# Optimization experiments

Hardware: AMD Instinct MI355X
Metric: run time of the kernel (lower is better)

The kernel has to match this reference:

```python
import jax, jax.numpy as jnp
import numpy as np

B, T, E, H = 4, 1024, 1024, 16
D = E // H  # head_size = 64
EPS = 1e-5


def layernorm(x, g, b):
    mu = jnp.mean(x, axis=-1, keepdims=True)
    var = jnp.mean(jnp.square(x - mu), axis=-1, keepdims=True)
    return (x - mu) * jax.lax.rsqrt(var + EPS) * g + b


def setup_inputs() -> dict:
    key = jax.random.key(0)
    ks = jax.random.split(key, 12)
    s = 0.02
    return {
        "x": jax.random.normal(ks[0], (B, T, E), dtype=jnp.float32),
        "ln1_g": jnp.ones((E,), jnp.float32),
        "ln1_b": jnp.zeros((E,), jnp.float32),
        "Wq": jax.random.normal(ks[1], (H, E, D), dtype=jnp.float32) * s,
        "Wk": jax.random.normal(ks[2], (H, E, D), dtype=jnp.float32) * s,
        "Wv": jax.random.normal(ks[3], (H, E, D), dtype=jnp.float32) * s,
        "Wp": jax.random.normal(ks[4], (E, E), dtype=jnp.float32) * s,
        "bp": jnp.zeros((E,), jnp.float32),
        "ln2_g": jnp.ones((E,), jnp.float32),
        "ln2_b": jnp.zeros((E,), jnp.float32),
        "W1": jax.random.normal(ks[5], (E, 4 * E), dtype=jnp.float32) * s,
        "b1": jnp.zeros((4 * E,), jnp.float32),
        "W2": jax.random.normal(ks[6], (4 * E, E), dtype=jnp.float32) * s,
        "b2": jnp.zeros((E,), jnp.float32),
    }


def reference(x, ln1_g, ln1_b, Wq, Wk, Wv, Wp, bp, ln2_g, ln2_b, W1, b1, W2, b2):
    # --- attention sub-block (pre-LN) ---
    h = layernorm(x, ln1_g, ln1_b)               # [B,T,E]
    q = jnp.einsum('bte,hed->bhtd', h, Wq)       # [B,H,T,D]
    k = jnp.einsum('bte,hed->bhtd', h, Wk)
    v = jnp.einsum('bte,hed->bhtd', h, Wv)
    # NOTE: original module has NO 1/sqrt(D) scaling and its 'tril' buffer is
    # all-ones, so masked_fill is a no-op -> full (non-causal) softmax.
    scores = jnp.einsum('bhtd,bhsd->bhts', q, k)  # [B,H,T,T]
    attn = jax.nn.softmax(scores, axis=-1)
    o = jnp.einsum('bhts,bhsd->bhtd', attn, v)    # [B,H,T,D]
    o = o.transpose(0, 2, 1, 3).reshape(x.shape[0], x.shape[1], -1)  # [B,T,E]
    x = x + o @ Wp + bp
    # --- feedforward sub-block (dropout is identity at eval) ---
    h2 = layernorm(x, ln2_g, ln2_b)
    x = x + jax.nn.relu(h2 @ W1 + b1) @ W2 + b2
    return x
```

## Files before the change

### kernel.cpp

```cpp
#include <hip/hip_runtime.h>
#include <hip/hip_bf16.h>

#define BB 4
#define TT 1024
#define EE 1024
#define HH 16
#define DD 64
#define MM 4096
#define NQKV 3072
#define E4 4096

using short8  = __attribute__((ext_vector_type(8))) short;
using short4v = __attribute__((ext_vector_type(4))) short;
using f32x4   = __attribute__((ext_vector_type(4))) float;

__device__ __forceinline__ short f2bf(float f) {
    __hip_bfloat16 h = __float2bfloat16(f);
    return *reinterpret_cast<short*>(&h);
}

__device__ __forceinline__ float bf2f(short s) {
    unsigned int u = ((unsigned int)(unsigned short)s) << 16;
    return __uint_as_float(u);
}

__device__ __forceinline__ unsigned int cvtpk_bf16(float a, float b) {
    unsigned int w;
    asm("v_cvt_pk_bf16_f32 %0, %1, %2" : "=v"(w) : "v"(a), "v"(b));
    return w;
}

__device__ __forceinline__ void gld16(const void* g, void* l) {
    __builtin_amdgcn_global_load_lds((__attribute__((address_space(1))) void*)g,
                                     (__attribute__((address_space(3))) void*)l,
                                     16, 0, 0);
}

__device__ __forceinline__ void tcvt_tile(const float* __restrict__ in,
                                          short* __restrict__ out,
                                          int R, int C, int r0, int c0) {
    __shared__ short tile[64][65];
    const int tr = threadIdx.x >> 6;
    const int tc = threadIdx.x & 63;
#pragma unroll
    for (int i = 0; i < 16; ++i) {
        int r = i * 4 + tr;
        tile[tc][r] = f2bf(in[(size_t)(r0 + r) * C + c0 + tc]);
    }
    __syncthreads();
#pragma unroll
    for (int i = 0; i < 16; ++i) {
        int c = i * 4 + tr;
        out[(size_t)(c0 + c) * R + r0 + tc] = tile[c][tc];
    }
}

__global__ __launch_bounds__(256) void packs_kernel(const float* __restrict__ Wq,
                                                    const float* __restrict__ Wk,
                                                    const float* __restrict__ Wv,
                                                    const float* __restrict__ Wp,
                                                    const float* __restrict__ W1,
                                                    const float* __restrict__ W2,
                                                    short* __restrict__ wqkv,
                                                    short* __restrict__ wp_bf,
                                                    short* __restrict__ w1_bf,
                                                    short* __restrict__ w2_bf) {
    const int blk = blockIdx.x;
    if (blk < 768) {
        __shared__ short tile[64][65];
        const int m = blk >> 4;
        const int which = m >> 4, head = m & 15;
        const float* src = ((which == 0) ? Wq : (which == 1) ? Wk : Wv) +
                           (size_t)head * EE * DD;
        const float scale = (which == 1) ? 1.44269504f : 1.0f;
        const int e0 = (blk & 15) * 64;
        const int tr = threadIdx.x >> 6, tc = threadIdx.x & 63;
#pragma unroll
        for (int i = 0; i < 16; ++i) {
            int e = i * 4 + tr;
            tile[tc][e] = f2bf(src[(size_t)(e0 + e) * DD + tc] * scale);
        }
        __syncthreads();
#pragma unroll
        for (int i = 0; i < 16; ++i) {
            int d = i * 4 + tr;
            wqkv[(size_t)(which * 1024 + head * 64 + d) * EE + e0 + tc] = tile[d][tc];
        }
    } else if (blk < 1024) {
        const int idx = blk - 768;
        tcvt_tile(Wp, wp_bf, EE, EE, (idx >> 4) * 64, (idx & 15) * 64);
    } else if (blk < 2048) {
        const int idx = blk - 1024;
        tcvt_tile(W1, w1_bf, EE, E4, (idx >> 6) * 64, (idx & 63) * 64);
    } else {
        const int idx = blk - 2048;
        tcvt_tile(W2, w2_bf, E4, EE, (idx >> 4) * 64, (idx & 15) * 64);
    }
}

__global__ __launch_bounds__(256) void vtr_kernel(const short* __restrict__ qkv,
                                                  short* __restrict__ vT) {
    __shared__ short tile[64][68];
    const int b = blockIdx.z;
    const int t0 = blockIdx.x * 64, c0 = blockIdx.y * 64;
    const int tr = threadIdx.x >> 4;
    const int q4 = (threadIdx.x & 15) * 4;
#pragma unroll
    for (int i = 0; i < 4; ++i) {
        int t = i * 16 + tr;
        short4v v = *(const short4v*)&qkv[((size_t)b * TT + t0 + t) * NQKV + 2048 + c0 + q4];
        *(short4v*)&tile[t][q4] = v;
    }
    __syncthreads();
#pragma unroll
    for (int i = 0; i < 4; ++i) {
        int c = i * 16 + tr;
        short4v v;
        v[0] = tile[q4 + 0][c];
        v[1] = tile[q4 + 1][c];
        v[2] = tile[q4 + 2][c];
        v[3] = tile[q4 + 3][c];
        *(short4v*)&vT[((size_t)b * 1024 + c0 + c) * TT + t0 + q4] = v;
    }
}

__global__ __launch_bounds__(256) void ln_kernel(const float* __restrict__ x,
                                                 const float* __restrict__ g,
                                                 const float* __restrict__ b,
                                                 short* __restrict__ out) {
    __shared__ float red[4];
    const int row = blockIdx.x;
    const int tid = threadIdx.x;
    float4 v = *(const float4*)&x[(size_t)row * EE + tid * 4];
    float s = v.x + v.y + v.z + v.w;
#pragma unroll
    for (int off = 32; off >= 1; off >>= 1) s += __shfl_xor(s, off, 64);
    if ((tid & 63) == 0) red[tid >> 6] = s;
    __syncthreads();
    float mean = (red[0] + red[1] + red[2] + red[3]) * (1.0f / EE);
    __syncthreads();
    float d0 = v.x - mean, d1 = v.y - mean, d2 = v.z - mean, d3 = v.w - mean;
    s = d0 * d0 + d1 * d1 + d2 * d2 + d3 * d3;
#pragma unroll
    for (int off = 32; off >= 1; off >>= 1) s += __shfl_xor(s, off, 64);
    if ((tid & 63) == 0) red[tid >> 6] = s;
    __syncthreads();
    float var = (red[0] + red[1] + red[2] + red[3]) * (1.0f / EE);
    float rstd = rsqrtf(var + 1e-5f);
    int c = tid * 4;
    short4v o;
    o[0] = f2bf(d0 * rstd * g[c + 0] + b[c + 0]);
    o[1] = f2bf(d1 * rstd * g[c + 1] + b[c + 1]);
    o[2] = f2bf(d2 * rstd * g[c + 2] + b[c + 2]);
    o[3] = f2bf(d3 * rstd * g[c + 3] + b[c + 3]);
    *(short4v*)&out[(size_t)row * EE + c] = o;
}

__global__ __launch_bounds__(256) void redk4_kernel(const short* __restrict__ parts,
                                                    const float* __restrict__ bias,
                                                    const float* __restrict__ resid,
                                                    float* __restrict__ out) {
    const size_t i = ((size_t)blockIdx.x * 256 + threadIdx.x) * 4;
    float4 r = *(const float4*)&resid[i];
    float4 bb = *(const float4*)&bias[i & 1023];
    float acc0 = r.x + bb.x, acc1 = r.y + bb.y, acc2 = r.z + bb.z, acc3 = r.w + bb.w;
#pragma unroll
    for (int z = 0; z < 4; ++z) {
        short4v p = *(const short4v*)&parts[(size_t)z * MM * EE + i];
        acc0 += bf2f(p[0]);
        acc1 += bf2f(p[1]);
        acc2 += bf2f(p[2]);
        acc3 += bf2f(p[3]);
    }
    float4 o;
    o.x = acc0; o.y = acc1; o.z = acc2; o.w = acc3;
    *(float4*)&out[i] = o;
}

template <bool HAS_BIAS, bool RELU, bool SPLIT>
__global__ __launch_bounds__(512, 2) void gemm256(const short* __restrict__ A,
                                                  const short* __restrict__ Bt,
                                                  const float* __restrict__ bias,
                                                  void* __restrict__ outp,
                                                  int M, int N, int K, int lda) {
    __shared__ __align__(16) short Ab[2][2][8192];
    __shared__ __align__(16) short Bb[2][2][8192];

    const int tid = threadIdx.x;
    const int lane = tid & 63;
    const int wid = tid >> 6;
    const int wr = wid >> 2;
    const int wc = wid & 3;
    const int l15 = lane & 15, lhi = lane >> 4;
    const int rsw = l15 & 7;

    int wg = blockIdx.y * gridDim.x + blockIdx.x;
    const int chunk = (gridDim.x * gridDim.y) >> 3;
    wg = (wg & 7) * chunk + (wg >> 3);
    const int bx = wg % gridDim.x, by = wg / gridDim.x;
    const int row0 = by * 256, col0 = bx * 256;

    const int kb = SPLIT ? blockIdx.z * K : 0;

    const int srow = tid >> 3;
    const int scol = (((tid & 7) ^ (srow & 7)) << 3);

    const int NT = K >> 6;

    f32x4 acc[8][4] = {};

    auto stageA = [&](int b, int h, int k0) {
#pragma unroll
        for (int j = 0; j < 2; ++j)
            gld16(&A[(size_t)(row0 + h * 128 + j * 64 + srow) * lda + kb + k0 + scol],
                  &Ab[b][h][j * 4096 + wid * 512]);
    };
    auto stageB = [&](int b, int h, int k0) {
#pragma unroll
        for (int j = 0; j < 2; ++j)
            gld16(&Bt[(size_t)(col0 + h * 128 + j * 64 + srow) * lda + kb + k0 + scol],
                  &Bb[b][h][j * 4096 + wid * 512]);
    };

    stageA(0, 0, 0); stageA(0, 1, 0);
    stageB(0, 0, 0); stageB(0, 1, 0);
    if (NT > 1) {
        stageB(1, 0, 64); stageB(1, 1, 64);
        asm volatile("s_waitcnt vmcnt(4)" ::: "memory");
    } else {
        asm volatile("s_waitcnt vmcnt(0)" ::: "memory");
    }
    __builtin_amdgcn_s_barrier();

    for (int u = 0; u < NT; ++u) {
        const int buf = u & 1;
        short8 bfr[4][2];
#pragma unroll
        for (int p = 0; p < 4; ++p) {
            if (p == 0) {
#pragma unroll
                for (int n = 0; n < 4; ++n)
#pragma unroll
                    for (int ks = 0; ks < 2; ++ks)
                        bfr[n][ks] = *(const short8*)&Bb[buf][wc >> 1]
                            [((wc & 1) * 64 + n * 16 + l15) * 64 +
                             (((ks << 2) + lhi) ^ rsw) * 8];
            }
            short8 af[2][2];
#pragma unroll
            for (int mi = 0; mi < 2; ++mi)
#pragma unroll
                for (int ks = 0; ks < 2; ++ks)
                    af[mi][ks] = *(const short8*)&Ab[buf][wr]
                        [((p * 2 + mi) * 16 + l15) * 64 +
                         (((ks << 2) + lhi) ^ rsw) * 8];
            if (p == 0 && u + 1 < NT) stageA(buf ^ 1, 0, (u + 1) << 6);
            if (p == 1 && u + 1 < NT) stageA(buf ^ 1, 1, (u + 1) << 6);
            if (p == 2 && u + 2 < NT) stageB(buf, 0, (u + 2) << 6);
            if (p == 3 && u + 2 < NT) stageB(buf, 1, (u + 2) << 6);
            __builtin_amdgcn_s_barrier();
            __builtin_amdgcn_s_setprio(1);
#pragma unroll
            for (int mi = 0; mi < 2; ++mi)
#pragma unroll
                for (int n = 0; n < 4; ++n)
#pragma unroll
                    for (int ks = 0; ks < 2; ++ks)
                        acc[p * 2 + mi][n] = __builtin_amdgcn_mfma_f32_16x16x32_bf16(
                            af[mi][ks], bfr[n][ks], acc[p * 2 + mi][n], 0, 0, 0);
            __builtin_amdgcn_s_setprio(0);
            if (p == 3 && u + 1 < NT) {
                if (u + 2 < NT) asm volatile("s_waitcnt vmcnt(4)" ::: "memory");
                else            asm volatile("s_waitcnt vmcnt(0)" ::: "memory");
            }
            __builtin_amdgcn_s_barrier();
        }
    }

    short* outb = (short*)outp;
    if (SPLIT) outb += (size_t)blockIdx.z * M * N;
#pragma unroll
    for (int m = 0; m < 8; ++m)
#pragma unroll
        for (int n = 0; n < 4; ++n)
#pragma unroll
            for (int r = 0; r < 4; ++r) {
                int row = row0 + wr * 128 + m * 16 + lhi * 4 + r;
                int col = col0 + wc * 64 + n * 16 + l15;
                float v = acc[m][n][r];
                if (!SPLIT) {
                    if (HAS_BIAS) v += bias[col];
                    if (RELU) v = fmaxf(v, 0.f);
                }
                outb[(size_t)row * N + col] = f2bf(v);
            }
}

template <int BN, int PIPE, bool HAS_BIAS, bool RELU, bool RESID, bool OUT_BF16>
__global__ __launch_bounds__(256) void gemm_bt(const short* __restrict__ A,
                                               const short* __restrict__ Bt,
                                               const float* __restrict__ bias,
                                               const float* __restrict__ resid,
                                               void* __restrict__ outp,
                                               int M, int N, int K) {
    constexpr int WRC = (BN == 128) ? 2 : 4;
    constexpr int WCC = (BN == 128) ? 2 : 1;
    constexpr int MI = 8 / WRC;
    constexpr int NI = BN / (16 * WCC);
    constexpr int BCH = BN / 32;
    constexpr int ASZ = 128 * 64, BSZ = BN * 64;

    __shared__ __align__(16) short As[(PIPE ? 2 : 1) * ASZ];
    __shared__ __align__(16) short Bs[(PIPE ? 2 : 1) * BSZ];

    const int tid = threadIdx.x;
    const int lane = tid & 63;
    const int wid = tid >> 6;
    const int wr = (WRC == 2) ? (wid >> 1) : wid;
    const int wc = (WCC == 2) ? (wid & 1) : 0;
    const int l15 = lane & 15, lhi = lane >> 4;

    int wg = blockIdx.y * gridDim.x + blockIdx.x;
    const int chunk = (gridDim.x * gridDim.y) >> 3;
    wg = (wg & 7) * chunk + (wg >> 3);
    const int bx = wg % gridDim.x;
    const int by = wg / gridDim.x;
    const int row0 = by * 128, col0 = bx * BN;

    const int srow = tid >> 3;
    const int scol = (((tid & 7) ^ (srow & 7)) << 3);
    const int rsw = l15 & 7;

    const int wrow0 = wr * (16 * MI);
    const int wcol0 = wc * (16 * NI);

    f32x4 acc[MI][NI] = {};

    auto stage = [&](int k0, int bs) {
#pragma unroll
        for (int ch = 0; ch < 4; ++ch)
            gld16(&A[(size_t)(row0 + ch * 32 + srow) * K + k0 + scol],
                  &As[bs * ASZ + ch * 2048 + wid * 512]);
#pragma unroll
        for (int ch = 0; ch < BCH; ++ch)
            gld16(&Bt[(size_t)(col0 + ch * 32 + srow) * K + k0 + scol],
                  &Bs[bs * BSZ + ch * 2048 + wid * 512]);
    };
    auto compute = [&](int bs) {
#pragma unroll
        for (int ks = 0; ks < 2; ++ks) {
            short8 af[MI], bf[NI];
#pragma unroll
            for (int mi = 0; mi < MI; ++mi)
                af[mi] = *(const short8*)&As[bs * ASZ + (wrow0 + mi * 16 + l15) * 64 +
                                             (((ks << 2) + lhi) ^ rsw) * 8];
#pragma unroll
            for (int ni = 0; ni < NI; ++ni)
                bf[ni] = *(const short8*)&Bs[bs * BSZ + (wcol0 + ni * 16 + l15) * 64 +
                                             (((ks << 2) + lhi) ^ rsw) * 8];
#pragma unroll
            for (int mi = 0; mi < MI; ++mi)
#pragma unroll
                for (int ni = 0; ni < NI; ++ni)
                    acc[mi][ni] = __builtin_amdgcn_mfma_f32_16x16x32_bf16(
                        af[mi], bf[ni], acc[mi][ni], 0, 0, 0);
        }
    };

    if (PIPE == 1) {
        const int nt = K >> 6;
        stage(0, 0);
        stage(64, 1);
        int cur = 0;
        for (int t = 0; t < nt; ++t) {
            if (t + 1 < nt) asm volatile("s_waitcnt vmcnt(6)" ::: "memory");
            else            asm volatile("s_waitcnt vmcnt(0)" ::: "memory");
            __builtin_amdgcn_s_barrier();
            __builtin_amdgcn_sched_barrier(0);
            compute(cur);
            __builtin_amdgcn_sched_barrier(0);
            __builtin_amdgcn_s_barrier();
            if (t + 2 < nt) stage((t + 2) << 6, cur);
            cur ^= 1;
        }
    } else {
        for (int k0 = 0; k0 < K; k0 += 64) {
            __syncthreads();
            stage(k0, 0);
            __syncthreads();
            compute(0);
        }
    }

    float* outf = (float*)outp;
    short* outb = (short*)outp;
#pragma unroll
    for (int mi = 0; mi < MI; ++mi)
#pragma unroll
        for (int ni = 0; ni < NI; ++ni)
#pragma unroll
            for (int r = 0; r < 4; ++r) {
                int row = row0 + wrow0 + mi * 16 + lhi * 4 + r;
                int col = col0 + wcol0 + ni * 16 + l15;
                float v = acc[mi][ni][r];
                if (HAS_BIAS) v += bias[col];
                if (RELU) v = fmaxf(v, 0.f);
                if (RESID) v += resid[(size_t)row * N + col];
                if (OUT_BF16) outb[(size_t)row * N + col] = f2bf(v);
                else outf[(size_t)row * N + col] = v;
            }
}

__global__ __launch_bounds__(512) void attn_kernel(const short* __restrict__ qkv,
                                                   const short* __restrict__ vT,
                                                   short* __restrict__ obuf) {
    __shared__ __align__(16) short Ks[2][128 * 64];
    __shared__ __align__(16) short Vs[2][64 * 128];
    __shared__ __align__(16) unsigned int Pl[8][16][44];
    const int tid = threadIdx.x;
    const int lane = tid & 63;
    const int wid = tid >> 6;
    const int l15 = lane & 15, lhi = lane >> 4;
    const int lhi4 = lhi * 4;

    const int nb = ((blockIdx.x & 7) << 5) + (blockIdx.x >> 3);
    const int b = nb >> 6;
    const int h = (nb >> 2) & 15;
    const int q0 = (nb & 3) << 8;
    const size_t rbase = (size_t)b * TT;
    const int hq = h * 64;
    const short* vg = vT + ((size_t)b * 1024 + hq) * TT;

    const int srow = tid >> 3;
    const int scol = (((tid & 7) ^ (srow & 7)) << 3);
    const int vrow = tid >> 4;
    const int vscol = ((tid & 15) ^ (vrow & 7)) << 3;
    const int rsw = l15 & 7;

    short8 aq[2][2];
#pragma unroll
    for (int g = 0; g < 2; ++g)
#pragma unroll
        for (int ks = 0; ks < 2; ++ks)
            aq[g][ks] = *(const short8*)&qkv[(rbase + q0 + wid * 32 + g * 16 + l15) * NQKV +
                                             hq + ks * 32 + lhi * 8];

    f32x4 psum[2] = {};
    f32x4 o[2][4] = {};

    auto stage = [&](int buf, int st) {
#pragma unroll
        for (int ch = 0; ch < 2; ++ch)
            gld16(&qkv[(rbase + st + ch * 64 + srow) * NQKV + 1024 + hq + scol],
                  &Ks[buf][ch * 4096 + wid * 512]);
#pragma unroll
        for (int ch = 0; ch < 2; ++ch)
            gld16(&vg[(size_t)(ch * 32 + vrow) * TT + st + vscol],
                  &Vs[buf][ch * 4096 + wid * 512]);
    };

    stage(0, 0);
    __syncthreads();

    int cur = 0;
    for (int st = 0; st < TT; st += 128) {
        if (st + 128 < TT) stage(cur ^ 1, st + 128);
        const short* K = &Ks[cur][0];
        const short* V = &Vs[cur][0];

#pragma unroll
        for (int h2 = 0; h2 < 2; ++h2) {
            short8 kf[4][2];
#pragma unroll
            for (int nt = 0; nt < 4; ++nt)
#pragma unroll
                for (int ks = 0; ks < 2; ++ks)
                    kf[nt][ks] = *(const short8*)&K[(h2 * 64 + nt * 16 + l15) * 64 +
                                                   (((ks << 2) + lhi) ^ rsw) * 8];

            short8 pa[2][2];
#pragma unroll
            for (int g = 0; g < 2; ++g) {
                f32x4 stv[4] = {};
                __builtin_amdgcn_s_setprio(1);
#pragma unroll
                for (int nt = 0; nt < 4; ++nt)
#pragma unroll
                    for (int ks = 0; ks < 2; ++ks)
                        stv[nt] = __builtin_amdgcn_mfma_f32_16x16x32_bf16(
                            kf[nt][ks], aq[g][ks], stv[nt], 0, 0, 0);
                __builtin_amdgcn_s_setprio(0);
#pragma unroll
                for (int nt = 0; nt < 4; ++nt) {
                    f32x4 pv;
#pragma unroll
                    for (int r = 0; r < 4; ++r) pv[r] = exp2f(stv[nt][r]);
                    psum[g] += pv;
                    uint2 ww;
                    ww.x = cvtpk_bf16(pv[0], pv[1]);
                    ww.y = cvtpk_bf16(pv[2], pv[3]);
                    *(uint2*)&Pl[wid][l15][nt * 8 + lhi * 2] = ww;
                }
                pa[g][0] = *(const short8*)&Pl[wid][l15][lhi4];
                pa[g][1] = *(const short8*)&Pl[wid][l15][16 + lhi4];
            }

            short8 vf[4][2];
#pragma unroll
            for (int dt = 0; dt < 4; ++dt)
#pragma unroll
                for (int k2 = 0; k2 < 2; ++k2)
                    vf[dt][k2] = *(const short8*)&V[(dt * 16 + l15) * 128 +
                                                   ((h2 << 3) + (((k2 << 2) + lhi) ^ rsw)) * 8];
            __builtin_amdgcn_s_setprio(1);
#pragma unroll
            for (int g = 0; g < 2; ++g)
#pragma unroll
                for (int dt = 0; dt < 4; ++dt)
#pragma unroll
                    for (int k2 = 0; k2 < 2; ++k2)
                        o[g][dt] = __builtin_amdgcn_mfma_f32_16x16x32_bf16(
                            pa[g][k2], vf[dt][k2], o[g][dt], 0, 0, 0);
            __builtin_amdgcn_s_setprio(0);
        }

        __syncthreads();
        cur ^= 1;
    }
#pragma unroll
    for (int g = 0; g < 2; ++g) {
        float ls = (psum[g][0] + psum[g][1]) + (psum[g][2] + psum[g][3]);
        ls += __shfl_xor(ls, 16, 64);
        ls += __shfl_xor(ls, 32, 64);
        float inv = 1.0f / ls;
        float i0 = __shfl(inv, lhi4 + 0, 64);
        float i1 = __shfl(inv, lhi4 + 1, 64);
        float i2 = __shfl(inv, lhi4 + 2, 64);
        float i3 = __shfl(inv, lhi4 + 3, 64);
#pragma unroll
        for (int dt = 0; dt < 4; ++dt) {
            int col = hq + dt * 16 + l15;
            size_t rw = rbase + q0 + wid * 32 + g * 16 + lhi4;
            obuf[(rw + 0) * EE + col] = f2bf(o[g][dt][0] * i0);
            obuf[(rw + 1) * EE + col] = f2bf(o[g][dt][1] * i1);
            obuf[(rw + 2) * EE + col] = f2bf(o[g][dt][2] * i2);
            obuf[(rw + 3) * EE + col] = f2bf(o[g][dt][3] * i3);
        }
    }
}

extern "C" void kernel_launch(void* const* d_in, const int* in_sizes, int n_in,
                              void* d_out, int out_size, void* d_ws, size_t ws_size,
                              hipStream_t stream) {
    const float* x   = (const float*)d_in[0];
    const float* g1  = (const float*)d_in[1];
    const float* be1 = (const float*)d_in[2];
    const float* Wq  = (const float*)d_in[3];
    const float* Wk  = (const float*)d_in[4];
    const float* Wv  = (const float*)d_in[5];
    const float* Wp  = (const float*)d_in[6];
    const float* bp  = (const float*)d_in[7];
    const float* g2  = (const float*)d_in[8];
    const float* be2 = (const float*)d_in[9];
    const float* W1  = (const float*)d_in[10];
    const float* b1f = (const float*)d_in[11];
    const float* W2  = (const float*)d_in[12];
    const float* b2f = (const float*)d_in[13];

    char* p = (char*)d_ws;
    short* h_bf   = (short*)p; p += (size_t)MM * EE * 2;
    short* wqkv   = (short*)p; p += (size_t)EE * NQKV * 2;
    short* qkv    = (short*)p; p += (size_t)MM * NQKV * 2;
    short* o_bf   = (short*)p; p += (size_t)MM * EE * 2;
    short* wp_bf  = (short*)p; p += (size_t)EE * EE * 2;
    float* x1     = (float*)p; p += (size_t)MM * EE * 4;
    short* h2_bf  = (short*)p; p += (size_t)MM * EE * 2;
    short* w1_bf  = (short*)p; p += (size_t)EE * E4 * 2;
    short* mid_bf = (short*)p; p += (size_t)MM * E4 * 2;
    short* w2_bf  = (short*)p; p += (size_t)E4 * EE * 2;
    short* vTb    = (short*)p; p += (size_t)BB * 1024 * TT * 2;

    short* parts = (short*)d_ws;

    packs_kernel<<<3072, 256, 0, stream>>>(Wq, Wk, Wv, Wp, W1, W2,
                                           wqkv, wp_bf, w1_bf, w2_bf);

    ln_kernel<<<MM, 256, 0, stream>>>(x, g1, be1, h_bf);

    gemm256<false, false, false>
        <<<dim3(NQKV / 256, MM / 256), 512, 0, stream>>>(h_bf, wqkv, nullptr,
                                                         qkv, MM, NQKV, EE, EE);

    vtr_kernel<<<dim3(16, 16, BB), 256, 0, stream>>>(qkv, vTb);

    attn_kernel<<<BB * HH * (TT / 256), 512, 0, stream>>>(qkv, vTb, o_bf);

    gemm_bt<64, 1, true, false, true, false>
        <<<dim3(EE / 64, MM / 128), 256, 0, stream>>>(o_bf, wp_bf, bp, x, x1, MM, EE, EE);

    ln_kernel<<<MM, 256, 0, stream>>>(x1, g2, be2, h2_bf);

    gemm256<true, true, false>
        <<<dim3(E4 / 256, MM / 256), 512, 0, stream>>>(h2_bf, w1_bf, b1f,
                                                       mid_bf, MM, E4, EE, EE);

    gemm256<false, false, true>
        <<<dim3(EE / 256, MM / 256, 4), 512, 0, stream>>>(mid_bf, w2_bf, nullptr,
                                                          parts, MM, EE, 1024, E4);
    redk4_kernel<<<(MM * EE / 4) / 256, 256, 0, stream>>>(parts, b2f, x1,
                                                          (float*)d_out);
}
```

Before: 199.7 us.

## Vectorize weight pack and split-K reduce, batch attention score MFMAs

Rewrites the transpose-convert helper so it uses float4 loads and short4 stores, and routes the QKV weight packing through it. The split-K reduction kernel now handles 8 elements per thread with wider loads and launches half as many blocks. In attention, both query groups' score MFMAs are issued back to back before the exp and pack step, and the P scratch buffer is doubled per group so the two groups no longer share it. This trades more registers and LDS in attention for better MFMA issue density. The transposed-tile LDS writes now use strided scalar stores, which may cause bank conflicts.

```diff
diff --git a/kernel.cpp b/kernel.cpp
--- a/kernel.cpp
+++ b/kernel.cpp
@@ -38,20 +38,26 @@
 
 __device__ __forceinline__ void tcvt_tile(const float* __restrict__ in,
                                           short* __restrict__ out,
-                                          int R, int C, int r0, int c0) {
-    __shared__ short tile[64][65];
-    const int tr = threadIdx.x >> 6;
-    const int tc = threadIdx.x & 63;
-#pragma unroll
-    for (int i = 0; i < 16; ++i) {
-        int r = i * 4 + tr;
-        tile[tc][r] = f2bf(in[(size_t)(r0 + r) * C + c0 + tc]);
+                                          int R, int C, int r0, int c0,
+                                          float scale) {
+    __shared__ short tile[64][68];
+    const int rr = threadIdx.x >> 4;
+    const int c4 = (threadIdx.x & 15) * 4;
+#pragma unroll
+    for (int i = 0; i < 4; ++i) {
+        int r = i * 16 + rr;
+        float4 v = *(const float4*)&in[(size_t)(r0 + r) * C + c0 + c4];
+        tile[c4 + 0][r] = f2bf(v.x * scale);
+        tile[c4 + 1][r] = f2bf(v.y * scale);
+        tile[c4 + 2][r] = f2bf(v.z * scale);
+        tile[c4 + 3][r] = f2bf(v.w * scale);
     }
     __syncthreads();
 #pragma unroll
-    for (int i = 0; i < 16; ++i) {
-        int c = i * 4 + tr;
-        out[(size_t)(c0 + c) * R + r0 + tc] = tile[c][tc];
+    for (int i = 0; i < 4; ++i) {
+        int c = i * 16 + rr;
+        short4v s = *(const short4v*)&tile[c][c4];
+        *(short4v*)&out[(size_t)(c0 + c) * R + r0 + c4] = s;
     }
 }
 
@@ -67,34 +73,23 @@
                                                     short* __restrict__ w2_bf) {
     const int blk = blockIdx.x;
     if (blk < 768) {
-        __shared__ short tile[64][65];
         const int m = blk >> 4;
         const int which = m >> 4, head = m & 15;
         const float* src = ((which == 0) ? Wq : (which == 1) ? Wk : Wv) +
                            (size_t)head * EE * DD;
         const float scale = (which == 1) ? 1.44269504f : 1.0f;
         const int e0 = (blk & 15) * 64;
-        const int tr = threadIdx.x >> 6, tc = threadIdx.x & 63;
-#pragma unroll
-        for (int i = 0; i < 16; ++i) {
-            int e = i * 4 + tr;
-            tile[tc][e] = f2bf(src[(size_t)(e0 + e) * DD + tc] * scale);
-        }
-        __syncthreads();
-#pragma unroll
-        for (int i = 0; i < 16; ++i) {
-            int d = i * 4 + tr;
-            wqkv[(size_t)(which * 1024 + head * 64 + d) * EE + e0 + tc] = tile[d][tc];
-        }
+        tcvt_tile(src, wqkv + (size_t)(which * 1024 + head * 64) * EE,
+                  EE, DD, e0, 0, scale);
     } else if (blk < 1024) {
         const int idx = blk - 768;
-        tcvt_tile(Wp, wp_bf, EE, EE, (idx >> 4) * 64, (idx & 15) * 64);
+        tcvt_tile(Wp, wp_bf, EE, EE, (idx >> 4) * 64, (idx & 15) * 64, 1.0f);
     } else if (blk < 2048) {
         const int idx = blk - 1024;
-        tcvt_tile(W1, w1_bf, EE, E4, (idx >> 6) * 64, (idx & 63) * 64);
+        tcvt_tile(W1, w1_bf, EE, E4, (idx >> 6) * 64, (idx & 63) * 64, 1.0f);
     } else {
         const int idx = blk - 2048;
-        tcvt_tile(W2, w2_bf, E4, EE, (idx >> 4) * 64, (idx & 15) * 64);
+        tcvt_tile(W2, w2_bf, E4, EE, (idx >> 4) * 64, (idx & 15) * 64, 1.0f);
     }
 }
 
@@ -160,21 +155,28 @@
                                                     const float* __restrict__ bias,
                                                     const float* __restrict__ resid,
                                                     float* __restrict__ out) {
-    const size_t i = ((size_t)blockIdx.x * 256 + threadIdx.x) * 4;
-    float4 r = *(const float4*)&resid[i];
-    float4 bb = *(const float4*)&bias[i & 1023];
-    float acc0 = r.x + bb.x, acc1 = r.y + bb.y, acc2 = r.z + bb.z, acc3 = r.w + bb.w;
+    const size_t i = ((size_t)blockIdx.x * 256 + threadIdx.x) * 8;
+    float4 r0 = *(const float4*)&resid[i];
+    float4 r1 = *(const float4*)&resid[i + 4];
+    const float* bb = &bias[i & 1023];
+    float4 b0 = *(const float4*)&bb[0];
+    float4 b1 = *(const float4*)&bb[4];
+    float acc[8];
+    acc[0] = r0.x + b0.x; acc[1] = r0.y + b0.y;
+    acc[2] = r0.z + b0.z; acc[3] = r0.w + b0.w;
+    acc[4] = r1.x + b1.x; acc[5] = r1.y + b1.y;
+    acc[6] = r1.z + b1.z; acc[7] = r1.w + b1.w;
 #pragma unroll
     for (int z = 0; z < 4; ++z) {
-        short4v p = *(const short4v*)&parts[(size_t)z * MM * EE + i];
-        acc0 += bf2f(p[0]);
-        acc1 += bf2f(p[1]);
-        acc2 += bf2f(p[2]);
-        acc3 += bf2f(p[3]);
-    }
-    float4 o;
-    o.x = acc0; o.y = acc1; o.z = acc2; o.w = acc3;
-    *(float4*)&out[i] = o;
+        short8 p = *(const short8*)&parts[(size_t)z * MM * EE + i];
+#pragma unroll
+        for (int j = 0; j < 8; ++j) acc[j] += bf2f(p[j]);
+    }
+    float4 o0, o1;
+    o0.x = acc[0]; o0.y = acc[1]; o0.z = acc[2]; o0.w = acc[3];
+    o1.x = acc[4]; o1.y = acc[5]; o1.z = acc[6]; o1.w = acc[7];
+    *(float4*)&out[i] = o0;
+    *(float4*)&out[i + 4] = o1;
 }
 
 template <bool HAS_BIAS, bool RELU, bool SPLIT>
@@ -416,7 +418,7 @@
                                                    short* __restrict__ obuf) {
     __shared__ __align__(16) short Ks[2][128 * 64];
     __shared__ __align__(16) short Vs[2][64 * 128];
-    __shared__ __align__(16) unsigned int Pl[8][16][44];
+    __shared__ __align__(16) unsigned int Pl[8][2][16][44];
     const int tid = threadIdx.x;
     const int lane = tid & 63;
     const int wid = tid >> 6;
@@ -478,31 +480,34 @@
                     kf[nt][ks] = *(const short8*)&K[(h2 * 64 + nt * 16 + l15) * 64 +
                                                    (((ks << 2) + lhi) ^ rsw) * 8];
 
+            f32x4 stv[2][4] = {};
+            __builtin_amdgcn_s_setprio(1);
+#pragma unroll
+            for (int g = 0; g < 2; ++g)
+#pragma unroll
+                for (int nt = 0; nt < 4; ++nt)
+#pragma unroll
+                    for (int ks = 0; ks < 2; ++ks)
+                        stv[g][nt] = __builtin_amdgcn_mfma_f32_16x16x32_bf16(
+                            kf[nt][ks], aq[g][ks], stv[g][nt], 0, 0, 0);
+            __builtin_amdgcn_s_setprio(0);
+
             short8 pa[2][2];
 #pragma unroll
             for (int g = 0; g < 2; ++g) {
-                f32x4 stv[4] = {};
-                __builtin_amdgcn_s_setprio(1);
-#pragma unroll
-                for (int nt = 0; nt < 4; ++nt)
-#pragma unroll
-                    for (int ks = 0; ks < 2; ++ks)
-                        stv[nt] = __builtin_amdgcn_mfma_f32_16x16x32_bf16(
-                            kf[nt][ks], aq[g][ks], stv[nt], 0, 0, 0);
-                __builtin_amdgcn_s_setprio(0);
 #pragma unroll
                 for (int nt = 0; nt < 4; ++nt) {
                     f32x4 pv;
 #pragma unroll
-                    for (int r = 0; r < 4; ++r) pv[r] = exp2f(stv[nt][r]);
+                    for (int r = 0; r < 4; ++r) pv[r] = exp2f(stv[g][nt][r]);
                     psum[g] += pv;
                     uint2 ww;
                     ww.x = cvtpk_bf16(pv[0], pv[1]);
                     ww.y = cvtpk_bf16(pv[2], pv[3]);
-                    *(uint2*)&Pl[wid][l15][nt * 8 + lhi * 2] = ww;
+                    *(uint2*)&Pl[wid][g][l15][nt * 8 + lhi * 2] = ww;
                 }
-                pa[g][0] = *(const short8*)&Pl[wid][l15][lhi4];
-                pa[g][1] = *(const short8*)&Pl[wid][l15][16 + lhi4];
+                pa[g][0] = *(const short8*)&Pl[wid][g][l15][lhi4];
+                pa[g][1] = *(const short8*)&Pl[wid][g][l15][16 + lhi4];
             }
 
             short8 vf[4][2];
@@ -607,6 +612,6 @@
     gemm256<false, false, true>
         <<<dim3(EE / 256, MM / 256, 4), 512, 0, stream>>>(mid_bf, w2_bf, nullptr,
                                                           parts, MM, EE, 1024, E4);
-    redk4_kernel<<<(MM * EE / 4) / 256, 256, 0, stream>>>(parts, b2f, x1,
+    redk4_kernel<<<(MM * EE / 8) / 256, 256, 0, stream>>>(parts, b2f, x1,
                                                           (float*)d_out);
 }
```

Measured after the change: 198.7 us, median of 2. About the same (-0.5%).
